# Kernel tuning notes

Hardware: AMD Instinct MI355X
Metric: run time of the kernel (lower is better)

Reference implementation:

```python
import jax, jax.numpy as jnp
import numpy as np

N, E, G, D, FIN, L, ELAB = 150000, 600000, 8192, 128, 16, 4, 500000
BN_EPS = 1e-5


def _bn(h, g, b, rm, rv):
    # eval-mode BatchNorm1d with running stats
    return (h - rm) * g * jax.lax.rsqrt(rv + BN_EPS) + b


def _pool_max(h, batch):
    # global_max_pool; empty segments -> 0 (instead of -inf)
    p = jax.ops.segment_max(h, batch, num_segments=G)
    return jnp.where(jnp.isneginf(p), 0.0, p)


def setup_inputs() -> dict:
    key = jax.random.key(0)
    ks = jax.random.split(key, 24)
    s_in = 1.0 / np.sqrt(FIN)
    s_d = 1.0 / np.sqrt(D)
    inp = {
        "x": jax.random.normal(ks[0], (N, FIN), jnp.float32),
        "edge_index": jax.random.randint(ks[1], (2, E), 0, N, jnp.int32),
        "batch": jnp.sort(jax.random.randint(ks[2], (N,), 0, G, jnp.int32)),
        "edge_index_labeled": jax.random.randint(ks[3], (2, ELAB), 0, G, jnp.int32),
        "edge_label": jax.random.randint(ks[4], (ELAB,), 0, 2, jnp.int32),
        # initial node encoder + initial linear (num_classes == emb_sizes == D)
        "enc_W": jax.random.normal(ks[5], (FIN, D), jnp.float32) * s_in,
        "enc_b": jnp.zeros((D,), jnp.float32),
        "init_W": jax.random.normal(ks[6], (D, D), jnp.float32) * s_d,
        "init_b": jnp.zeros((D,), jnp.float32),
        # per-layer GIN params (stacked over L layers)
        "gin_eps": jnp.zeros((L,), jnp.float32),
        "W1": jax.random.normal(ks[7], (L, D, D), jnp.float32) * s_d,
        "b1": jnp.zeros((L, D), jnp.float32),
        "g1": jnp.ones((L, D), jnp.float32),
        "be1": jnp.zeros((L, D), jnp.float32),
        "rm1": jnp.zeros((L, D), jnp.float32),
        "rv1": jnp.ones((L, D), jnp.float32),
        "W2": jax.random.normal(ks[8], (L, D, D), jnp.float32) * s_d,
        "b2": jnp.zeros((L, D), jnp.float32),
        "g2": jnp.ones((L, D), jnp.float32),
        "be2": jnp.zeros((L, D), jnp.float32),
        "rm2": jnp.zeros((L, D), jnp.float32),
        "rv2": jnp.ones((L, D), jnp.float32),
        # per-layer linear applied to pooled features
        "lin_W": jax.random.normal(ks[9], (L, D, D), jnp.float32) * s_d,
        "lin_b": jnp.zeros((L, D), jnp.float32),
        # layer_post_mp: ReLU -> Linear(D,D) -> ReLU -> Linear(D,1)
        "post_W1": jax.random.normal(ks[10], (D, D), jnp.float32) * s_d,
        "post_b1": jnp.zeros((D,), jnp.float32),
        "post_W2": jax.random.normal(ks[11], (D, 1), jnp.float32) * s_d,
        "post_b2": jnp.zeros((1,), jnp.float32),
    }
    return inp


def reference(x, edge_index, batch, edge_index_labeled, edge_label,
              enc_W, enc_b, init_W, init_b, gin_eps,
              W1, b1, g1, be1, rm1, rv1,
              W2, b2, g2, be2, rm2, rv2,
              lin_W, lin_b, post_W1, post_b1, post_W2, post_b2):
    src, dst = edge_index[0], edge_index[1]

    # initial MLP (node encoder) -> [N, D]
    x_feat = x @ enc_W + enc_b

    # out = dropout(pool(initial_linear(x_feat)))  (dropout = identity, eval)
    out = _pool_max(x_feat @ init_W + init_b, batch)  # [G, D]

    for i in range(L):
        # GINConv: mlp((1 + eps) * x + sum_{j in N(i)} x_j)
        agg = jax.ops.segment_sum(x_feat[src], dst, num_segments=N)  # [N, D]
        h = (1.0 + gin_eps[i]) * x_feat + agg
        h = jax.nn.relu(_bn(h @ W1[i] + b1[i], g1[i], be1[i], rm1[i], rv1[i]))
        x_feat = jax.nn.relu(_bn(h @ W2[i] + b2[i], g2[i], be2[i], rm2[i], rv2[i]))
        # out += dropout(linear(pool(x_feat)))
        out = out + (_pool_max(x_feat, batch) @ lin_W[i] + lin_b[i])

    # layer_post_mp: ReLU -> Linear -> ReLU -> Linear(D,1)
    out = jax.nn.relu(out)
    out = jax.nn.relu(out @ post_W1 + post_b1)
    out = out @ post_W2 + post_b2  # [G, 1]

    # _apply_index gather + dot-product decode
    pred_pairs = out[edge_index_labeled]  # [2, ELAB, 1]
    pred = jnp.sum(pred_pairs[0] * pred_pairs[1], axis=-1)  # [ELAB]
    return pred, edge_label
```

## Files before the change

### kernel.cpp

```cpp
#include <hip/hip_runtime.h>

#define NN 150000
#define NP 150016
#define NE 600000
#define NG 8192
#define DD 128
#define FINN 16
#define NL 4
#define NEL 500000
#define BN_EPS 1e-5f
#define NB_SCAN 147

typedef __attribute__((ext_vector_type(8))) short bf16x8;
typedef __attribute__((ext_vector_type(4))) float f32x4;

__device__ inline short bfr(float x) {
    unsigned u = __builtin_bit_cast(unsigned, x);
    unsigned r = u + 0x7fffu + ((u >> 16) & 1u);
    return (short)(r >> 16);
}
__device__ inline float bf2f(short h) {
    return __builtin_bit_cast(float, ((unsigned)(unsigned short)h) << 16);
}

__global__ void enc_kernel(const float* __restrict__ x, const float* __restrict__ W,
                           const float* __restrict__ b, float* __restrict__ out) {
    int tid = blockIdx.x * blockDim.x + threadIdx.x;
    if (tid >= NN * DD) return;
    int n = tid >> 7, d = tid & 127;
    float acc = b[d];
    const float* xr = x + n * FINN;
#pragma unroll
    for (int k = 0; k < FINN; k++) acc += xr[k] * W[k * DD + d];
    out[tid] = acc;
}

__global__ void prep_w_kernel(const float* __restrict__ initW, const float* __restrict__ W1,
                              const float* __restrict__ W2, bf16x8* __restrict__ Wph,
                              bf16x8* __restrict__ Wpl) {
    int tid = blockIdx.x * 256 + threadIdx.x;
    if (tid >= 9 * 2048) return;
    int mat = tid >> 11;
    int rem = tid & 2047;
    int kk = rem >> 9;
    int c = (rem >> 6) & 7;
    int lane = rem & 63;
    const float* Wm;
    if (mat == 0) Wm = initW;
    else if (mat <= 4) Wm = W1 + (size_t)(mat - 1) * DD * DD;
    else Wm = W2 + (size_t)(mat - 5) * DD * DD;
    int col = c * 16 + (lane & 15);
    int kbase = kk * 32 + (lane >> 4) * 8;
    bf16x8 oh, ol;
#pragma unroll
    for (int j = 0; j < 8; j++) {
        float v = Wm[(size_t)(kbase + j) * DD + col];
        short h = bfr(v);
        oh[j] = h;
        ol[j] = bfr(v - bf2f(h));
    }
    Wph[tid] = oh;
    Wpl[tid] = ol;
}

__global__ void prep_scb_kernel(const float* __restrict__ initb,
                                const float* __restrict__ b1, const float* __restrict__ g1,
                                const float* __restrict__ be1, const float* __restrict__ rm1,
                                const float* __restrict__ rv1,
                                const float* __restrict__ b2, const float* __restrict__ g2,
                                const float* __restrict__ be2, const float* __restrict__ rm2,
                                const float* __restrict__ rv2,
                                float* __restrict__ sc, float* __restrict__ bb) {
    int tid = blockIdx.x * 256 + threadIdx.x;
    if (tid >= 9 * DD) return;
    int mat = tid >> 7, d = tid & 127;
    float s, o;
    if (mat == 0) {
        s = 1.f;
        o = initb[d];
    } else {
        const float *b_, *g_, *be_, *rm_, *rv_;
        int i;
        if (mat <= 4) { i = mat - 1; b_ = b1; g_ = g1; be_ = be1; rm_ = rm1; rv_ = rv1; }
        else          { i = mat - 5; b_ = b2; g_ = g2; be_ = be2; rm_ = rm2; rv_ = rv2; }
        float t = g_[i * DD + d] * rsqrtf(rv_[i * DD + d] + BN_EPS);
        s = t;
        o = (b_[i * DD + d] - rm_[i * DD + d]) * t + be_[i * DD + d];
    }
    sc[tid] = s;
    bb[tid] = o;
}

__global__ void zero_int_kernel(int* __restrict__ p, int n) {
    int i = blockIdx.x * 256 + threadIdx.x;
    if (i < n) p[i] = 0;
}

__global__ void hist_kernel(const int* __restrict__ dst, int* __restrict__ deg) {
    int e = blockIdx.x * 256 + threadIdx.x;
    if (e < NE) atomicAdd(&deg[dst[e]], 1);
}

__global__ void scan_reduce_kernel(const int* __restrict__ deg, int* __restrict__ bsum) {
    __shared__ int s[256];
    int b = blockIdx.x, t = threadIdx.x;
    int base = b * 1024 + t * 4;
    int v = 0;
#pragma unroll
    for (int i = 0; i < 4; i++) {
        int idx = base + i;
        if (idx < NN) v += deg[idx];
    }
    s[t] = v;
    __syncthreads();
    for (int off = 128; off > 0; off >>= 1) {
        if (t < off) s[t] += s[t + off];
        __syncthreads();
    }
    if (t == 0) bsum[b] = s[0];
}

__global__ void scan_mid_kernel(const int* __restrict__ bsum, int* __restrict__ boff,
                                int* __restrict__ rowptrN) {
    __shared__ int s[256];
    int t = threadIdx.x;
    int v = (t < NB_SCAN) ? bsum[t] : 0;
    s[t] = v;
    __syncthreads();
    for (int off = 1; off < 256; off <<= 1) {
        int u = (t >= off) ? s[t - off] : 0;
        __syncthreads();
        s[t] += u;
        __syncthreads();
    }
    if (t < NB_SCAN) boff[t] = s[t] - v;
    if (t == 255) *rowptrN = s[255];
}

__global__ void scan_final_kernel(const int* __restrict__ deg, const int* __restrict__ boff,
                                  int* __restrict__ rowptr) {
    __shared__ int s[256];
    int b = blockIdx.x, t = threadIdx.x;
    int base = b * 1024 + t * 4;
    int v[4];
    int sum = 0;
#pragma unroll
    for (int i = 0; i < 4; i++) {
        int idx = base + i;
        v[i] = (idx < NN) ? deg[idx] : 0;
        sum += v[i];
    }
    s[t] = sum;
    __syncthreads();
    int my = sum;
    for (int off = 1; off < 256; off <<= 1) {
        int u = (t >= off) ? s[t - off] : 0;
        __syncthreads();
        s[t] += u;
        __syncthreads();
    }
    int excl = s[t] - my + boff[b];
#pragma unroll
    for (int i = 0; i < 4; i++) {
        int idx = base + i;
        if (idx < NN) rowptr[idx] = excl;
        excl += v[i];
    }
}

__global__ void copy_int_kernel(const int* __restrict__ a, int* __restrict__ b, int n) {
    int i = blockIdx.x * 256 + threadIdx.x;
    if (i < n) b[i] = a[i];
}

__global__ void fill_kernel(const int* __restrict__ src, const int* __restrict__ dst,
                            int* cursor, int* __restrict__ csr_src) {
    int e = blockIdx.x * 256 + threadIdx.x;
    if (e >= NE) return;
    int p = atomicAdd(&cursor[dst[e]], 1);
    csr_src[p] = src[e];
}

__global__ void gstart_kernel(const int* __restrict__ batch, int* __restrict__ gstart) {
    int n = blockIdx.x * 256 + threadIdx.x;
    if (n >= NN) return;
    int b = batch[n];
    int prev = (n == 0) ? -1 : batch[n - 1];
    for (int g = prev + 1; g <= b; g++) gstart[g] = n;
    if (n == NN - 1) {
        for (int g = b + 1; g <= NG; g++) gstart[g] = NN;
    }
}

__global__ __launch_bounds__(256) void agg_kernel(const f32x4* __restrict__ A4,
                                                  const int* __restrict__ rowptr,
                                                  const int* __restrict__ csr_src,
                                                  const float* __restrict__ gin_eps,
                                                  int li, f32x4* __restrict__ B4) {
    int n = blockIdx.x * 8 + (threadIdx.x >> 5);
    int c = threadIdx.x & 31;
    float e1 = 1.f + gin_eps[li];
    int s = rowptr[n], e = rowptr[n + 1];
    int base = n << 5;
    f32x4 acc = A4[base + c] * e1;
    int i = s;
    for (; i + 4 <= e; i += 4) {
        int j0 = csr_src[i];
        int j1 = csr_src[i + 1];
        int j2 = csr_src[i + 2];
        int j3 = csr_src[i + 3];
        f32x4 v0 = A4[(j0 << 5) + c];
        f32x4 v1 = A4[(j1 << 5) + c];
        f32x4 v2 = A4[(j2 << 5) + c];
        f32x4 v3 = A4[(j3 << 5) + c];
        acc += (v0 + v1) + (v2 + v3);
    }
    for (; i < e; i++) acc += A4[(csr_src[i] << 5) + c];
    B4[base + c] = acc;
}

template <int RELU>
__global__ __launch_bounds__(256) void mm_kernel(const float* __restrict__ A,
                                                 float* __restrict__ C,
                                                 const bf16x8* __restrict__ Wph,
                                                 const bf16x8* __restrict__ Wpl,
                                                 const float* __restrict__ sc,
                                                 const float* __restrict__ bb) {
    int lane = threadIdx.x & 63;
    int wid = threadIdx.x >> 6;
    int row0 = blockIdx.x * 128 + wid * 32;
    int r16 = lane & 15;
    int kg = lane >> 4;
    f32x4 acc[2][8];
#pragma unroll
    for (int m = 0; m < 2; m++)
#pragma unroll
        for (int c = 0; c < 8; c++) acc[m][c] = (f32x4){0.f, 0.f, 0.f, 0.f};
#pragma unroll
    for (int kk = 0; kk < 4; kk++) {
        bf16x8 ah[2], al[2];
#pragma unroll
        for (int m = 0; m < 2; m++) {
            const float* ap = A + (size_t)(row0 + m * 16 + r16) * DD + kk * 32 + kg * 8;
            float4 lo = *(const float4*)ap;
            float4 hi = *(const float4*)(ap + 4);
            float v[8] = {lo.x, lo.y, lo.z, lo.w, hi.x, hi.y, hi.z, hi.w};
            bf16x8 th, tl;
#pragma unroll
            for (int j = 0; j < 8; j++) {
                short h = bfr(v[j]);
                th[j] = h;
                tl[j] = bfr(v[j] - bf2f(h));
            }
            ah[m] = th;
            al[m] = tl;
        }
#pragma unroll
        for (int c = 0; c < 8; c++) {
            bf16x8 wh = Wph[kk * 512 + c * 64 + lane];
            bf16x8 wl = Wpl[kk * 512 + c * 64 + lane];
#pragma unroll
            for (int m = 0; m < 2; m++) {
                acc[m][c] = __builtin_amdgcn_mfma_f32_16x16x32_bf16(ah[m], wh, acc[m][c], 0, 0, 0);
                acc[m][c] = __builtin_amdgcn_mfma_f32_16x16x32_bf16(al[m], wh, acc[m][c], 0, 0, 0);
                acc[m][c] = __builtin_amdgcn_mfma_f32_16x16x32_bf16(ah[m], wl, acc[m][c], 0, 0, 0);
            }
        }
    }
#pragma unroll
    for (int c = 0; c < 8; c++) {
        int col = c * 16 + r16;
        float s = sc[col], o = bb[col];
#pragma unroll
        for (int m = 0; m < 2; m++) {
            int rbase = row0 + m * 16 + kg * 4;
#pragma unroll
            for (int j = 0; j < 4; j++) {
                int row = rbase + j;
                if (row < NN) {
                    float v = acc[m][c][j] * s + o;
                    if (RELU) v = fmaxf(v, 0.f);
                    C[(size_t)row * DD + col] = v;
                }
            }
        }
    }
}

__global__ void pool0_kernel(const float* __restrict__ X, const int* __restrict__ gstart,
                             float* __restrict__ OUT) {
    int gph = blockIdx.x;
    int d = threadIdx.x;
    int start = gstart[gph], end = gstart[gph + 1];
    float m;
    if (start >= end) {
        m = 0.f;
    } else {
        m = -INFINITY;
        for (int n = start; n < end; n++) m = fmaxf(m, X[(size_t)n * DD + d]);
    }
    OUT[(size_t)gph * DD + d] = m;
}

__global__ __launch_bounds__(128) void poollin_kernel(const float* __restrict__ X,
                                                      const int* __restrict__ gstart,
                                                      const float* __restrict__ W,
                                                      const float* __restrict__ b,
                                                      float* __restrict__ OUT) {
    __shared__ float p[4][DD];
    int g0 = blockIdx.x * 4;
    int d = threadIdx.x;
#pragma unroll
    for (int gg = 0; gg < 4; gg++) {
        int start = gstart[g0 + gg], end = gstart[g0 + gg + 1];
        float m;
        if (start >= end) {
            m = 0.f;
        } else {
            m = -INFINITY;
            for (int n = start; n < end; n++) m = fmaxf(m, X[(size_t)n * DD + d]);
        }
        p[gg][d] = m;
    }
    __syncthreads();
    float acc0 = b[d], acc1 = b[d], acc2 = b[d], acc3 = b[d];
#pragma unroll 8
    for (int k = 0; k < DD; k++) {
        float w = W[k * DD + d];
        acc0 += p[0][k] * w;
        acc1 += p[1][k] * w;
        acc2 += p[2][k] * w;
        acc3 += p[3][k] * w;
    }
    OUT[(size_t)(g0 + 0) * DD + d] += acc0;
    OUT[(size_t)(g0 + 1) * DD + d] += acc1;
    OUT[(size_t)(g0 + 2) * DD + d] += acc2;
    OUT[(size_t)(g0 + 3) * DD + d] += acc3;
}

__global__ void post_kernel(const float* __restrict__ OUT, const float* __restrict__ W1,
                            const float* __restrict__ b1, const float* __restrict__ W2,
                            const float* __restrict__ b2, float* __restrict__ S) {
    __shared__ float o[DD];
    __shared__ float red[2];
    int gph = blockIdx.x, d = threadIdx.x;
    o[d] = fmaxf(OUT[(size_t)gph * DD + d], 0.f);
    __syncthreads();
    float acc = b1[d];
#pragma unroll 8
    for (int k = 0; k < DD; k++) acc += o[k] * W1[k * DD + d];
    acc = fmaxf(acc, 0.f);
    float v = acc * W2[d];
#pragma unroll
    for (int off = 32; off > 0; off >>= 1) v += __shfl_down(v, off);
    if ((d & 63) == 0) red[d >> 6] = v;
    __syncthreads();
    if (d == 0) S[gph] = red[0] + red[1] + b2[0];
}

__global__ void pred_kernel(const int* __restrict__ eil, const int* __restrict__ el,
                            const float* __restrict__ S, float* __restrict__ out) {
    int i = blockIdx.x * blockDim.x + threadIdx.x;
    if (i >= NEL) return;
    int a = eil[i], b = eil[NEL + i];
    out[i] = S[a] * S[b];
    out[NEL + i] = (float)el[i];
}

extern "C" void kernel_launch(void* const* d_in, const int* in_sizes, int n_in,
                              void* d_out, int out_size, void* d_ws, size_t ws_size,
                              hipStream_t stream) {
    const float* x = (const float*)d_in[0];
    const int* edge_index = (const int*)d_in[1];
    const int* batch = (const int*)d_in[2];
    const int* eil = (const int*)d_in[3];
    const int* el = (const int*)d_in[4];
    const float* encW = (const float*)d_in[5];
    const float* encb = (const float*)d_in[6];
    const float* initW = (const float*)d_in[7];
    const float* initb = (const float*)d_in[8];
    const float* gin_eps = (const float*)d_in[9];
    const float* W1 = (const float*)d_in[10];
    const float* b1 = (const float*)d_in[11];
    const float* g1 = (const float*)d_in[12];
    const float* be1 = (const float*)d_in[13];
    const float* rm1 = (const float*)d_in[14];
    const float* rv1 = (const float*)d_in[15];
    const float* W2 = (const float*)d_in[16];
    const float* b2 = (const float*)d_in[17];
    const float* g2 = (const float*)d_in[18];
    const float* be2 = (const float*)d_in[19];
    const float* rm2 = (const float*)d_in[20];
    const float* rv2 = (const float*)d_in[21];
    const float* linW = (const float*)d_in[22];
    const float* linb = (const float*)d_in[23];
    const float* postW1 = (const float*)d_in[24];
    const float* postb1 = (const float*)d_in[25];
    const float* postW2 = (const float*)d_in[26];
    const float* postb2 = (const float*)d_in[27];

    const int* srcArr = edge_index;
    const int* dstArr = edge_index + NE;

    char* w = (char*)d_ws;
    auto carve = [&](size_t bytes) -> char* {
        char* p = w;
        w += (bytes + 255) & ~(size_t)255;
        return p;
    };
    float* A = (float*)carve((size_t)NP * DD * 4);
    float* B = (float*)carve((size_t)NP * DD * 4);
    float* OUTb = (float*)carve((size_t)NG * DD * 4);
    float* S = (float*)carve((size_t)NG * 4);
    int* deg = (int*)carve((size_t)NN * 4);
    int* rowptr = (int*)carve((size_t)(NN + 1) * 4);
    int* cursor = (int*)carve((size_t)NN * 4);
    int* csr_src = (int*)carve((size_t)NE * 4);
    int* bsum = (int*)carve((size_t)NB_SCAN * 4);
    int* boff = (int*)carve((size_t)NB_SCAN * 4);
    int* gstart = (int*)carve((size_t)(NG + 1) * 4);
    bf16x8* Wph = (bf16x8*)carve((size_t)9 * 2048 * 16);
    bf16x8* Wpl = (bf16x8*)carve((size_t)9 * 2048 * 16);
    float* scv = (float*)carve((size_t)9 * DD * 4);
    float* bbv = (float*)carve((size_t)9 * DD * 4);

    float* out = (float*)d_out;
    const int mmBlk = NP / 128;

    prep_w_kernel<<<72, 256, 0, stream>>>(initW, W1, W2, Wph, Wpl);
    prep_scb_kernel<<<5, 256, 0, stream>>>(initb, b1, g1, be1, rm1, rv1,
                                           b2, g2, be2, rm2, rv2, scv, bbv);

    zero_int_kernel<<<586, 256, 0, stream>>>(deg, NN);
    hist_kernel<<<2344, 256, 0, stream>>>(dstArr, deg);
    scan_reduce_kernel<<<NB_SCAN, 256, 0, stream>>>(deg, bsum);
    scan_mid_kernel<<<1, 256, 0, stream>>>(bsum, boff, rowptr + NN);
    scan_final_kernel<<<NB_SCAN, 256, 0, stream>>>(deg, boff, rowptr);
    copy_int_kernel<<<586, 256, 0, stream>>>(rowptr, cursor, NN);
    fill_kernel<<<2344, 256, 0, stream>>>(srcArr, dstArr, cursor, csr_src);
    gstart_kernel<<<586, 256, 0, stream>>>(batch, gstart);

    enc_kernel<<<(NN * DD) / 256, 256, 0, stream>>>(x, encW, encb, A);
    mm_kernel<0><<<mmBlk, 256, 0, stream>>>(A, B, Wph, Wpl, scv, bbv);
    pool0_kernel<<<NG, DD, 0, stream>>>(B, gstart, OUTb);

    for (int i = 0; i < NL; i++) {
        agg_kernel<<<NN / 8, 256, 0, stream>>>((const f32x4*)A, rowptr, csr_src,
                                               gin_eps, i, (f32x4*)B);
        mm_kernel<1><<<mmBlk, 256, 0, stream>>>(B, B, Wph + (size_t)(1 + i) * 2048,
                                                Wpl + (size_t)(1 + i) * 2048,
                                                scv + (1 + i) * DD, bbv + (1 + i) * DD);
        mm_kernel<1><<<mmBlk, 256, 0, stream>>>(B, A, Wph + (size_t)(5 + i) * 2048,
                                                Wpl + (size_t)(5 + i) * 2048,
                                                scv + (5 + i) * DD, bbv + (5 + i) * DD);
        poollin_kernel<<<NG / 4, DD, 0, stream>>>(A, gstart, linW + (size_t)i * DD * DD,
                                                  linb + i * DD, OUTb);
    }

    post_kernel<<<NG, DD, 0, stream>>>(OUTb, postW1, postb1, postW2, postb2, S);
    pred_kernel<<<(NEL + 255) / 256, 256, 0, stream>>>(eil, el, S, out);
}
```

Before: 1.068 ms.

## Fuse GIN MLP's two matmuls through LDS; register-tile encoder

Each GIN layer's two matmul+BN+ReLU stages now run in one kernel. The intermediate 128x128 tile per block stays in shared memory with an XOR swizzle instead of making a round trip through global memory. This removes one kernel launch and a write plus read of an N x 128 fp32 buffer per layer, at the cost of 64KB of LDS per block, which lowers occupancy. The encoder kernel was also rewritten so each thread keeps weights in registers and computes float4 outputs across 16 rows with vectorized loads.

```diff
diff --git a/kernel.cpp b/kernel.cpp
--- a/kernel.cpp
+++ b/kernel.cpp
@@ -23,16 +23,35 @@
     return __builtin_bit_cast(float, ((unsigned)(unsigned short)h) << 16);
 }
 
-__global__ void enc_kernel(const float* __restrict__ x, const float* __restrict__ W,
-                           const float* __restrict__ b, float* __restrict__ out) {
-    int tid = blockIdx.x * blockDim.x + threadIdx.x;
-    if (tid >= NN * DD) return;
-    int n = tid >> 7, d = tid & 127;
-    float acc = b[d];
-    const float* xr = x + n * FINN;
-#pragma unroll
-    for (int k = 0; k < FINN; k++) acc += xr[k] * W[k * DD + d];
-    out[tid] = acc;
+__global__ __launch_bounds__(256) void enc_kernel(const float* __restrict__ x,
+                                                  const float* __restrict__ W,
+                                                  const float* __restrict__ b,
+                                                  float* __restrict__ out) {
+    int t = threadIdx.x;
+    int c4 = (t & 31) * 4;
+    float4 wreg[16];
+#pragma unroll
+    for (int k = 0; k < 16; k++) wreg[k] = *(const float4*)&W[k * DD + c4];
+    float4 bias = *(const float4*)&b[c4];
+    int rbase = blockIdx.x * 128 + (t >> 5);
+#pragma unroll
+    for (int it = 0; it < 16; it++) {
+        int row = rbase + it * 8;
+        if (row >= NN) break;
+        const float4* xr = (const float4*)(x + (size_t)row * FINN);
+        float4 x0 = xr[0], x1 = xr[1], x2 = xr[2], x3 = xr[3];
+        float xs[16] = {x0.x, x0.y, x0.z, x0.w, x1.x, x1.y, x1.z, x1.w,
+                        x2.x, x2.y, x2.z, x2.w, x3.x, x3.y, x3.z, x3.w};
+        float4 acc = bias;
+#pragma unroll
+        for (int k = 0; k < 16; k++) {
+            acc.x += xs[k] * wreg[k].x;
+            acc.y += xs[k] * wreg[k].y;
+            acc.z += xs[k] * wreg[k].z;
+            acc.w += xs[k] * wreg[k].w;
+        }
+        *(float4*)&out[(size_t)row * DD + c4] = acc;
+    }
 }
 
 __global__ void prep_w_kernel(const float* __restrict__ initW, const float* __restrict__ W1,
@@ -281,6 +300,126 @@
                     float v = acc[m][c][j] * s + o;
                     if (RELU) v = fmaxf(v, 0.f);
                     C[(size_t)row * DD + col] = v;
+                }
+            }
+        }
+    }
+}
+
+__global__ __launch_bounds__(256) void mm2x_kernel(
+    const float* __restrict__ Ain, float* __restrict__ Aout,
+    const bf16x8* __restrict__ Wph1, const bf16x8* __restrict__ Wpl1,
+    const bf16x8* __restrict__ Wph2, const bf16x8* __restrict__ Wpl2,
+    const float* __restrict__ sc1, const float* __restrict__ bb1,
+    const float* __restrict__ sc2, const float* __restrict__ bb2) {
+    __shared__ float hl[128 * 128];
+    int lane = threadIdx.x & 63;
+    int wid = threadIdx.x >> 6;
+    int row0 = blockIdx.x * 128 + wid * 32;
+    int r16 = lane & 15;
+    int kg = lane >> 4;
+    f32x4 acc[2][8];
+#pragma unroll
+    for (int m = 0; m < 2; m++)
+#pragma unroll
+        for (int c = 0; c < 8; c++) acc[m][c] = (f32x4){0.f, 0.f, 0.f, 0.f};
+
+#pragma unroll
+    for (int kk = 0; kk < 4; kk++) {
+        bf16x8 ah[2], al[2];
+#pragma unroll
+        for (int m = 0; m < 2; m++) {
+            const float* ap = Ain + (size_t)(row0 + m * 16 + r16) * DD + kk * 32 + kg * 8;
+            float4 lo = *(const float4*)ap;
+            float4 hi = *(const float4*)(ap + 4);
+            float v[8] = {lo.x, lo.y, lo.z, lo.w, hi.x, hi.y, hi.z, hi.w};
+            bf16x8 th, tl;
+#pragma unroll
+            for (int j = 0; j < 8; j++) {
+                short h = bfr(v[j]);
+                th[j] = h;
+                tl[j] = bfr(v[j] - bf2f(h));
+            }
+            ah[m] = th;
+            al[m] = tl;
+        }
+#pragma unroll
+        for (int c = 0; c < 8; c++) {
+            bf16x8 wh = Wph1[kk * 512 + c * 64 + lane];
+            bf16x8 wl = Wpl1[kk * 512 + c * 64 + lane];
+#pragma unroll
+            for (int m = 0; m < 2; m++) {
+                acc[m][c] = __builtin_amdgcn_mfma_f32_16x16x32_bf16(ah[m], wh, acc[m][c], 0, 0, 0);
+                acc[m][c] = __builtin_amdgcn_mfma_f32_16x16x32_bf16(al[m], wh, acc[m][c], 0, 0, 0);
+                acc[m][c] = __builtin_amdgcn_mfma_f32_16x16x32_bf16(ah[m], wl, acc[m][c], 0, 0, 0);
+            }
+        }
+    }
+#pragma unroll
+    for (int c = 0; c < 8; c++) {
+        int col = c * 16 + r16;
+        float s = sc1[col], o = bb1[col];
+#pragma unroll
+        for (int m = 0; m < 2; m++) {
+#pragma unroll
+            for (int j = 0; j < 4; j++) {
+                int rl = wid * 32 + m * 16 + kg * 4 + j;
+                float v = fmaxf(acc[m][c][j] * s + o, 0.f);
+                hl[rl * 128 + (col ^ ((rl & 7) << 2))] = v;
+            }
+        }
+    }
+    __syncthreads();
+
+#pragma unroll
+    for (int m = 0; m < 2; m++)
+#pragma unroll
+        for (int c = 0; c < 8; c++) acc[m][c] = (f32x4){0.f, 0.f, 0.f, 0.f};
+#pragma unroll
+    for (int kk = 0; kk < 4; kk++) {
+        bf16x8 ah[2], al[2];
+#pragma unroll
+        for (int m = 0; m < 2; m++) {
+            int rl = wid * 32 + m * 16 + r16;
+            int sw = (rl & 7) << 2;
+            int c0 = kk * 32 + kg * 8;
+            float4 lo = *(const float4*)&hl[rl * 128 + (c0 ^ sw)];
+            float4 hi = *(const float4*)&hl[rl * 128 + ((c0 + 4) ^ sw)];
+            float v[8] = {lo.x, lo.y, lo.z, lo.w, hi.x, hi.y, hi.z, hi.w};
+            bf16x8 th, tl;
+#pragma unroll
+            for (int j = 0; j < 8; j++) {
+                short h = bfr(v[j]);
+                th[j] = h;
+                tl[j] = bfr(v[j] - bf2f(h));
+            }
+            ah[m] = th;
+            al[m] = tl;
+        }
+#pragma unroll
+        for (int c = 0; c < 8; c++) {
+            bf16x8 wh = Wph2[kk * 512 + c * 64 + lane];
+            bf16x8 wl = Wpl2[kk * 512 + c * 64 + lane];
+#pragma unroll
+            for (int m = 0; m < 2; m++) {
+                acc[m][c] = __builtin_amdgcn_mfma_f32_16x16x32_bf16(ah[m], wh, acc[m][c], 0, 0, 0);
+                acc[m][c] = __builtin_amdgcn_mfma_f32_16x16x32_bf16(al[m], wh, acc[m][c], 0, 0, 0);
+                acc[m][c] = __builtin_amdgcn_mfma_f32_16x16x32_bf16(ah[m], wl, acc[m][c], 0, 0, 0);
+            }
+        }
+    }
+#pragma unroll
+    for (int c = 0; c < 8; c++) {
+        int col = c * 16 + r16;
+        float s = sc2[col], o = bb2[col];
+#pragma unroll
+        for (int m = 0; m < 2; m++) {
+            int rbase = row0 + m * 16 + kg * 4;
+#pragma unroll
+            for (int j = 0; j < 4; j++) {
+                int row = rbase + j;
+                if (row < NN) {
+                    Aout[(size_t)row * DD + col] = fmaxf(acc[m][c][j] * s + o, 0.f);
                 }
             }
         }
@@ -440,19 +579,19 @@
     fill_kernel<<<2344, 256, 0, stream>>>(srcArr, dstArr, cursor, csr_src);
     gstart_kernel<<<586, 256, 0, stream>>>(batch, gstart);
 
-    enc_kernel<<<(NN * DD) / 256, 256, 0, stream>>>(x, encW, encb, A);
+    enc_kernel<<<mmBlk, 256, 0, stream>>>(x, encW, encb, A);
     mm_kernel<0><<<mmBlk, 256, 0, stream>>>(A, B, Wph, Wpl, scv, bbv);
     pool0_kernel<<<NG, DD, 0, stream>>>(B, gstart, OUTb);
 
     for (int i = 0; i < NL; i++) {
         agg_kernel<<<NN / 8, 256, 0, stream>>>((const f32x4*)A, rowptr, csr_src,
                                                gin_eps, i, (f32x4*)B);
-        mm_kernel<1><<<mmBlk, 256, 0, stream>>>(B, B, Wph + (size_t)(1 + i) * 2048,
-                                                Wpl + (size_t)(1 + i) * 2048,
-                                                scv + (1 + i) * DD, bbv + (1 + i) * DD);
-        mm_kernel<1><<<mmBlk, 256, 0, stream>>>(B, A, Wph + (size_t)(5 + i) * 2048,
-                                                Wpl + (size_t)(5 + i) * 2048,
-                                                scv + (5 + i) * DD, bbv + (5 + i) * DD);
+        mm2x_kernel<<<mmBlk, 256, 0, stream>>>(
+            B, A,
+            Wph + (size_t)(1 + i) * 2048, Wpl + (size_t)(1 + i) * 2048,
+            Wph + (size_t)(5 + i) * 2048, Wpl + (size_t)(5 + i) * 2048,
+            scv + (1 + i) * DD, bbv + (1 + i) * DD,
+            scv + (5 + i) * DD, bbv + (5 + i) * DD);
         poollin_kernel<<<NG / 4, DD, 0, stream>>>(A, gstart, linW + (size_t)i * DD * DD,
                                                   linb + i * DD, OUTb);
     }
```

Result: faster. 1.018 ms (-4.7%).
